# Performance work log

Hardware: AMD Instinct MI355X
Metric: run time of the kernel (lower is better)

Reference implementation:

```python
import jax, jax.numpy as jnp
import numpy as np

D_NIBBLE = 16
NIBBLE_VALUES = 16
NUM_NIBBLES = 8


def _build_tables():
    num_entries = NIBBLE_VALUES * NIBBLE_VALUES * 2  # 512
    input_dim = 2 * D_NIBBLE + 2                     # 34
    W1 = np.zeros((input_dim, num_entries), dtype=np.float32)
    W2_sum = np.zeros((num_entries, D_NIBBLE), dtype=np.float32)
    W2_carry = np.zeros((num_entries, 2), dtype=np.float32)
    for a in range(NIBBLE_VALUES):
        for b in range(NIBBLE_VALUES):
            for c in range(2):
                k = a * 32 + b * 2 + c
                W1[a, k] = 1.0
                W1[D_NIBBLE + b, k] = 1.0
                W1[2 * D_NIBBLE + c, k] = 1.0
                total = a + b + c
                W2_sum[k, total % 16] = 1.0
                W2_carry[k, 1 if total >= 16 else 0] = 1.0
    return jnp.asarray(W1), jnp.asarray(W2_sum), jnp.asarray(W2_carry)


def setup_inputs() -> dict:
    key = jax.random.key(0)
    k1, k2 = jax.random.split(key)
    B = 32768
    a_nibbles = jax.random.uniform(k1, (B, NUM_NIBBLES, 32), dtype=jnp.float32)
    b_nibbles = jax.random.uniform(k2, (B, NUM_NIBBLES, 32), dtype=jnp.float32)
    W1, W2_sum, W2_carry = _build_tables()
    threshold = jnp.float32(2.5)
    return {"a_nibbles": a_nibbles, "b_nibbles": b_nibbles,
            "W1": W1, "W2_sum": W2_sum, "W2_carry": W2_carry,
            "threshold": threshold}


def reference(a_nibbles, b_nibbles, W1, W2_sum, W2_carry, threshold):
    # a_nibbles, b_nibbles: [B, 8, 32]; first 16 feats = value one-hot, rest = pos
    B = a_nibbles.shape[0]
    carry0 = jnp.zeros((B, 2), a_nibbles.dtype).at[:, 0].set(1.0)  # carry=0 one-hot
    a_steps = jnp.swapaxes(a_nibbles, 0, 1)  # [8, B, 32]
    b_steps = jnp.swapaxes(b_nibbles, 0, 1)

    def step(carry, ab):
        a, b = ab  # [B, 32] each
        x = jnp.concatenate([a[:, :D_NIBBLE], b[:, :D_NIBBLE], carry], axis=-1)  # [B,34]
        scores = x @ W1                                     # [B,512]
        weights = jax.nn.softmax((scores - threshold) * 10.0, axis=-1)
        result = weights @ W2_sum                           # [B,16]
        new_carry = weights @ W2_carry                      # [B,2]
        out = jnp.concatenate([result, a[:, D_NIBBLE:]], axis=-1)  # [B,32]
        return new_carry, out

    _, outs = jax.lax.scan(step, carry0, (a_steps, b_steps))  # outs: [8, B, 32]
    return jnp.swapaxes(outs, 0, 1)  # [B, 8, 32]
```

## Files before the change

kernel.cpp:

```cpp
#include <hip/hip_runtime.h>


#define LOG2E10 14.426950408889634f

#if __has_builtin(__builtin_amdgcn_exp2f)
#define EXP2F(x) __builtin_amdgcn_exp2f(x)
#else
#define EXP2F(x) exp2f(x)
#endif

#if __has_builtin(__builtin_amdgcn_rcpf)
#define RCPF(x) __builtin_amdgcn_rcpf(x)
#else
#define RCPF(x) (1.0f / (x))
#endif

#define LSTRIDE 17

__global__ __launch_bounds__(64) void AdditionFFN_kernel(
    const float* __restrict__ A, const float* __restrict__ Bv,
    float* __restrict__ O, int nRows)
{
    __shared__ float sa[64 * LSTRIDE];
    __shared__ float sb[64 * LSTRIDE];
    __shared__ float sr[64 * LSTRIDE];

    const int L = threadIdx.x;
    const int r0 = blockIdx.x * 64;
    if (r0 >= nRows) return;

    float ec0 = EXP2F(LOG2E10);
    float ec1 = 1.0f;

    for (int s = 0; s < 8; ++s) {
        const int so = s * 32;

        #pragma unroll
        for (int q = 0; q < 4; ++q) {
            int f = q * 64 + L;
            int row = f >> 2;
            int c = f & 3;
            size_t g = (size_t)(r0 + row) * 256 + so + c * 4;
            float4 va = *(const float4*)(A + g);
            float4 vb = *(const float4*)(Bv + g);
            float* da = &sa[row * LSTRIDE + c * 4];
            da[0] = va.x; da[1] = va.y; da[2] = va.z; da[3] = va.w;
            float* db = &sb[row * LSTRIDE + c * 4];
            db[0] = vb.x; db[1] = vb.y; db[2] = vb.z; db[3] = vb.w;
            float4 vp = *(const float4*)(A + g + 16);
            *(float4*)(O + g + 16) = vp;
        }
        __syncthreads();

        float ea[16], eb[16];
        #pragma unroll
        for (int j = 0; j < 16; ++j) {
            ea[j] = EXP2F(sa[L * LSTRIDE + j] * LOG2E10);
            eb[j] = EXP2F(sb[L * LSTRIDE + j] * LOG2E10);
        }

        float u[31];
        #pragma unroll
        for (int t = 0; t < 31; ++t) u[t] = 0.0f;
        #pragma unroll
        for (int a = 0; a < 16; ++a) {
            #pragma unroll
            for (int b = 0; b < 16; ++b) {
                u[a + b] = __builtin_fmaf(ea[a], eb[b], u[a + b]);
            }
        }

        float sa0 = 0.f, sa1 = 0.f, sb0 = 0.f, sb1 = 0.f;
        #pragma unroll
        for (int t = 0; t < 16; t += 2) {
            sa0 += ea[t]; sa1 += ea[t + 1];
            sb0 += eb[t]; sb1 += eb[t + 1];
        }
        float Z = (sa0 + sa1) * (sb0 + sb1) * (ec0 + ec1);
        float rZ = RCPF(Z);
        rZ = rZ * (2.0f - Z * rZ);

        float hi0 = 0.0f;
        #pragma unroll
        for (int t = 16; t < 31; ++t) hi0 += u[t];
        float hi1 = hi0 + u[15];
        float carry1 = (ec0 * hi0 + ec1 * hi1) * rZ;
        carry1 = fminf(fmaxf(carry1, 0.0f), 1.0f);
        float carry0 = 1.0f - carry1;

        float res[16];
        #pragma unroll
        for (int j = 0; j < 16; ++j) {
            float t0 = u[j] * ec0 + ((j > 0) ? u[j - 1] * ec1 : 0.0f);
            float t1 = ((j < 15) ? u[j + 16] * ec0 : 0.0f) + u[j + 15] * ec1;
            res[j] = (t0 + t1) * rZ;
        }

        ec0 = EXP2F(carry0 * LOG2E10);
        ec1 = EXP2F(carry1 * LOG2E10);

        #pragma unroll
        for (int j = 0; j < 16; ++j) sr[L * LSTRIDE + j] = res[j];
        __syncthreads();

        #pragma unroll
        for (int q = 0; q < 4; ++q) {
            int f = q * 64 + L;
            int row = f >> 2;
            int c = f & 3;
            size_t g = (size_t)(r0 + row) * 256 + so + c * 4;
            const float* sp = &sr[row * LSTRIDE + c * 4];
            float4 r;
            r.x = sp[0]; r.y = sp[1]; r.z = sp[2]; r.w = sp[3];
            *(float4*)(O + g) = r;
        }
        __syncthreads();
    }
}

extern "C" void kernel_launch(void* const* d_in, const int* in_sizes, int n_in,
                              void* d_out, int out_size, void* d_ws, size_t ws_size,
                              hipStream_t stream) {
    (void)n_in; (void)out_size; (void)d_ws; (void)ws_size;
    const int nRows = in_sizes[0] / 256;
    const float* A  = (const float*)d_in[0];
    const float* Bv = (const float*)d_in[1];
    float* O = (float*)d_out;
    int blocks = (nRows + 63) / 64;
    AdditionFFN_kernel<<<blocks, 64, 0, stream>>>(A, Bv, O, nRows);
}
```

Baseline: 117.8 us.

## Split each row across four lanes with shuffles and register prefetch

Each row is now handled by a quad of four threads instead of one. Each lane loads its own float4 slice directly from global memory, and the lanes exchange exponentials with width-4 shuffles. Each lane computes only its four output sums of the convolution, and the totals are combined with xor-shuffle reductions. The shared-memory staging and barriers are removed, and the next step's inputs are prefetched into registers. This quarters the per-thread FMA work and raises occupancy and parallelism, at the cost of shuffle traffic and some redundant work across lanes.

```diff
diff --git a/kernel.cpp b/kernel.cpp
--- a/kernel.cpp
+++ b/kernel.cpp
@@ -15,106 +15,110 @@
 #define RCPF(x) (1.0f / (x))
 #endif
 
-#define LSTRIDE 17
+#define EBZ(x) ebz[(x) + 12]
 
-__global__ __launch_bounds__(64) void AdditionFFN_kernel(
-    const float* __restrict__ A, const float* __restrict__ Bv,
-    float* __restrict__ O, int nRows)
+__global__ __launch_bounds__(256) void AdditionFFN_kernel(
+    const float4* __restrict__ A, const float4* __restrict__ Bv,
+    float4* __restrict__ O, int nRows)
 {
-    __shared__ float sa[64 * LSTRIDE];
-    __shared__ float sb[64 * LSTRIDE];
-    __shared__ float sr[64 * LSTRIDE];
-
-    const int L = threadIdx.x;
-    const int r0 = blockIdx.x * 64;
-    if (r0 >= nRows) return;
+    const int T = threadIdx.x;
+    const int c = T & 3;
+    const int row = blockIdx.x * 64 + (T >> 2);
+    if (row >= nRows) return;
+    const float4* a4 = A + (size_t)row * 64;
+    const float4* b4 = Bv + (size_t)row * 64;
+    float4* o4 = O + (size_t)row * 64;
 
     float ec0 = EXP2F(LOG2E10);
     float ec1 = 1.0f;
 
+    float4 av = a4[c], bv = b4[c], pv = a4[4 + c];
+
     for (int s = 0; s < 8; ++s) {
-        const int so = s * 32;
+        const int sn = (s < 7) ? (s + 1) : 7;
+        float4 n_av = a4[sn * 8 + c];
+        float4 n_bv = b4[sn * 8 + c];
+        float4 n_pv = a4[sn * 8 + 4 + c];
 
+        o4[s * 8 + 4 + c] = pv;
+
+        float ea_own[4] = { EXP2F(av.x * LOG2E10), EXP2F(av.y * LOG2E10),
+                            EXP2F(av.z * LOG2E10), EXP2F(av.w * LOG2E10) };
+        float eb_own[4] = { EXP2F(bv.x * LOG2E10), EXP2F(bv.y * LOG2E10),
+                            EXP2F(bv.z * LOG2E10), EXP2F(bv.w * LOG2E10) };
+
+        float ea[16];
         #pragma unroll
-        for (int q = 0; q < 4; ++q) {
-            int f = q * 64 + L;
-            int row = f >> 2;
-            int c = f & 3;
-            size_t g = (size_t)(r0 + row) * 256 + so + c * 4;
-            float4 va = *(const float4*)(A + g);
-            float4 vb = *(const float4*)(Bv + g);
-            float* da = &sa[row * LSTRIDE + c * 4];
-            da[0] = va.x; da[1] = va.y; da[2] = va.z; da[3] = va.w;
-            float* db = &sb[row * LSTRIDE + c * 4];
-            db[0] = vb.x; db[1] = vb.y; db[2] = vb.z; db[3] = vb.w;
-            float4 vp = *(const float4*)(A + g + 16);
-            *(float4*)(O + g + 16) = vp;
-        }
-        __syncthreads();
-
-        float ea[16], eb[16];
-        #pragma unroll
-        for (int j = 0; j < 16; ++j) {
-            ea[j] = EXP2F(sa[L * LSTRIDE + j] * LOG2E10);
-            eb[j] = EXP2F(sb[L * LSTRIDE + j] * LOG2E10);
-        }
-
-        float u[31];
-        #pragma unroll
-        for (int t = 0; t < 31; ++t) u[t] = 0.0f;
-        #pragma unroll
-        for (int a = 0; a < 16; ++a) {
+        for (int k = 0; k < 4; ++k) {
             #pragma unroll
-            for (int b = 0; b < 16; ++b) {
-                u[a + b] = __builtin_fmaf(ea[a], eb[b], u[a + b]);
+            for (int m = 0; m < 4; ++m) {
+                ea[4 * k + m] = __shfl(ea_own[m], k, 4);
             }
         }
 
-        float sa0 = 0.f, sa1 = 0.f, sb0 = 0.f, sb1 = 0.f;
+        float ebz[28];
         #pragma unroll
-        for (int t = 0; t < 16; t += 2) {
-            sa0 += ea[t]; sa1 += ea[t + 1];
-            sb0 += eb[t]; sb1 += eb[t + 1];
+        for (int x = -12; x <= 15; ++x) {
+            int g = x + 4 * c;
+            float vsh = __shfl(eb_own[x & 3], (g >> 2) & 3, 4);
+            EBZ(x) = ((unsigned)g <= 15u) ? vsh : 0.0f;
         }
-        float Z = (sa0 + sa1) * (sb0 + sb1) * (ec0 + ec1);
+
+        float ulo[5], uhi[5];
+        #pragma unroll
+        for (int i = 0; i < 5; ++i) {
+            float acc = 0.0f;
+            const int amax = (i + 11 < 15) ? (i + 11) : 15;
+            #pragma unroll
+            for (int a = 0; a <= amax; ++a) {
+                acc = __builtin_fmaf(ea[a], EBZ(i - 1 - a), acc);
+            }
+            ulo[i] = acc;
+        }
+        #pragma unroll
+        for (int i = 0; i < 5; ++i) {
+            float acc = 0.0f;
+            #pragma unroll
+            for (int a = i; a < 16; ++a) {
+                acc = __builtin_fmaf(ea[a], EBZ(i + 15 - a), acc);
+            }
+            uhi[i] = acc;
+        }
+
+        float Sa = 0.0f;
+        #pragma unroll
+        for (int k = 0; k < 16; ++k) Sa += ea[k];
+        float sbp = (eb_own[0] + eb_own[1]) + (eb_own[2] + eb_own[3]);
+        sbp += __shfl_xor(sbp, 1, 4);
+        sbp += __shfl_xor(sbp, 2, 4);
+        const float E = ec0 + ec1;
+        float Z = Sa * sbp * E;
         float rZ = RCPF(Z);
         rZ = rZ * (2.0f - Z * rZ);
 
-        float hi0 = 0.0f;
-        #pragma unroll
-        for (int t = 16; t < 31; ++t) hi0 += u[t];
-        float hi1 = hi0 + u[15];
-        float carry1 = (ec0 * hi0 + ec1 * hi1) * rZ;
+        float hi0p = (uhi[1] + uhi[2]) + (uhi[3] + uhi[4]);
+        float phi = hi0p * E + ((c == 0) ? uhi[0] * ec1 : 0.0f);
+        phi += __shfl_xor(phi, 1, 4);
+        phi += __shfl_xor(phi, 2, 4);
+        float carry1 = phi * rZ;
         carry1 = fminf(fmaxf(carry1, 0.0f), 1.0f);
         float carry0 = 1.0f - carry1;
 
-        float res[16];
-        #pragma unroll
-        for (int j = 0; j < 16; ++j) {
-            float t0 = u[j] * ec0 + ((j > 0) ? u[j - 1] * ec1 : 0.0f);
-            float t1 = ((j < 15) ? u[j + 16] * ec0 : 0.0f) + u[j + 15] * ec1;
-            res[j] = (t0 + t1) * rZ;
-        }
+        float vm1 = ulo[0] + uhi[0];
+        float v0 = ulo[1] + uhi[1];
+        float v1 = ulo[2] + uhi[2];
+        float v2 = ulo[3] + uhi[3];
+        float v3 = ulo[4] + uhi[4];
+        float4 r;
+        r.x = (v0 * ec0 + vm1 * ec1) * rZ;
+        r.y = (v1 * ec0 + v0 * ec1) * rZ;
+        r.z = (v2 * ec0 + v1 * ec1) * rZ;
+        r.w = (v3 * ec0 + v2 * ec1) * rZ;
+        o4[s * 8 + c] = r;
 
         ec0 = EXP2F(carry0 * LOG2E10);
         ec1 = EXP2F(carry1 * LOG2E10);
-
-        #pragma unroll
-        for (int j = 0; j < 16; ++j) sr[L * LSTRIDE + j] = res[j];
-        __syncthreads();
-
-        #pragma unroll
-        for (int q = 0; q < 4; ++q) {
-            int f = q * 64 + L;
-            int row = f >> 2;
-            int c = f & 3;
-            size_t g = (size_t)(r0 + row) * 256 + so + c * 4;
-            const float* sp = &sr[row * LSTRIDE + c * 4];
-            float4 r;
-            r.x = sp[0]; r.y = sp[1]; r.z = sp[2]; r.w = sp[3];
-            *(float4*)(O + g) = r;
-        }
-        __syncthreads();
+        av = n_av; bv = n_bv; pv = n_pv;
     }
 }
 
@@ -123,9 +127,9 @@
                               hipStream_t stream) {
     (void)n_in; (void)out_size; (void)d_ws; (void)ws_size;
     const int nRows = in_sizes[0] / 256;
-    const float* A  = (const float*)d_in[0];
-    const float* Bv = (const float*)d_in[1];
-    float* O = (float*)d_out;
+    const float4* A  = (const float4*)d_in[0];
+    const float4* Bv = (const float4*)d_in[1];
+    float4* O = (float4*)d_out;
     int blocks = (nRows + 63) / 64;
-    AdditionFFN_kernel<<<blocks, 64, 0, stream>>>(A, Bv, O, nRows);
+    AdditionFFN_kernel<<<blocks, 256, 0, stream>>>(A, Bv, O, nRows);
 }
```

After: 116.3 us. About the same (-1.3%).
